# Kernel tuning notes

Measured on AMD Instinct MI355X. Metric: run time of the kernel, lower is better.

The kernel has to match this reference:

```python
import jax, jax.numpy as jnp
import numpy as np

N = 50000
E = 600000
IN_C = 128
OUT_C = 64
HID = 2 * OUT_C  # 128


def setup_inputs() -> dict:
    key = jax.random.key(0)
    ks = jax.random.split(key, 8)
    x = jax.random.normal(ks[0], (N, IN_C), dtype=jnp.float32)
    edge_index = jax.random.randint(ks[1], (2, E), 0, N, dtype=jnp.int64)
    # Glorot-style init for GCN weights, zero bias (PyG default)
    def glorot(k, fan_in, fan_out):
        s = jnp.sqrt(6.0 / (fan_in + fan_out)).astype(jnp.float32)
        return jax.random.uniform(k, (fan_in, fan_out), jnp.float32, -s, s)
    return {
        "x": x,
        "edge_index": edge_index,
        "W1": glorot(ks[2], IN_C, HID),
        "b1": jnp.zeros((HID,), jnp.float32),
        "W_mu": glorot(ks[3], HID, OUT_C),
        "b_mu": jnp.zeros((OUT_C,), jnp.float32),
        "W_ls": glorot(ks[4], HID, OUT_C),
        "b_ls": jnp.zeros((OUT_C,), jnp.float32),
    }


def _gcn_norm(edge_index, num_nodes):
    # Add self-loops, compute symmetric normalization (cached=True in original
    # means this is computed once and reused by all three convs -- same math).
    loop = jnp.arange(num_nodes, dtype=edge_index.dtype)
    row = jnp.concatenate([edge_index[0], loop])  # source
    col = jnp.concatenate([edge_index[1], loop])  # target
    deg = jax.ops.segment_sum(jnp.ones_like(col, dtype=jnp.float32), col,
                              num_segments=num_nodes)
    dis = jnp.where(deg > 0, jax.lax.rsqrt(deg), 0.0)  # deg^{-1/2}, inf->0
    norm = dis[row] * dis[col]  # [E+N]
    return row, col, norm


def _gcn_conv(x, W, b, row, col, norm, num_nodes):
    h = x @ W                                  # dense transform [N, out]
    msg = h[row] * norm[:, None]               # gather + scale [E+N, out]
    out = jax.ops.segment_sum(msg, col, num_segments=num_nodes)
    return out + b


def reference(x, edge_index, W1, b1, W_mu, b_mu, W_ls, b_ls):
    num_nodes = x.shape[0]
    row, col, norm = _gcn_norm(edge_index, num_nodes)
    # eval mode: F.dropout is identity when not training
    h = jax.nn.relu(_gcn_conv(x, W1, b1, row, col, norm, num_nodes))
    mu = _gcn_conv(h, W_mu, b_mu, row, col, norm, num_nodes)
    logstd = _gcn_conv(h, W_ls, b_ls, row, col, norm, num_nodes)
    return mu, logstd
```

## Files before the change

kernel.cpp:

```cpp
#include <hip/hip_runtime.h>
#include <hip/hip_fp16.h>


#define N_NODES 50000
#define N_EDGES 600000
#define MU_SIZE (N_NODES * 64)
#define SCAN_BLOCKS 200
#define SCAN_CHUNK 250
#define WT_S 136

typedef _Float16 half8 __attribute__((ext_vector_type(8)));
typedef _Float16 half4 __attribute__((ext_vector_type(4)));
typedef float floatx4 __attribute__((ext_vector_type(4)));

union H8 { __half2 h2[4]; float4 f4; };

__global__ __launch_bounds__(256) void count_kernel(const int* __restrict__ col,
                                                    int* __restrict__ counts, int e) {
  int i = blockIdx.x * 256 + threadIdx.x;
  if (i < e) atomicAdd(&counts[col[i]], 1);
}

__global__ __launch_bounds__(256) void blocksum_dis_kernel(const int* __restrict__ counts,
                                                           float* __restrict__ dis,
                                                           int* __restrict__ blocksums) {
  __shared__ int red[4];
  int b = blockIdx.x, t = threadIdx.x;
  int i = b * SCAN_CHUNK + t;
  int c = 0;
  if (t < SCAN_CHUNK) {
    c = counts[i];
    dis[i] = rsqrtf((float)(c + 1));
  }
  int s = c;
#pragma unroll
  for (int off = 32; off > 0; off >>= 1) s += __shfl_down(s, off, 64);
  if ((t & 63) == 0) red[t >> 6] = s;
  __syncthreads();
  if (t == 0) blocksums[b] = red[0] + red[1] + red[2] + red[3];
}

__global__ __launch_bounds__(256) void offsets_kernel(const int* __restrict__ counts,
                                                      const int* __restrict__ blocksums,
                                                      int* __restrict__ offsets) {
  __shared__ int sb[256];
  __shared__ int loc[256];
  int b = blockIdx.x, t = threadIdx.x;
  sb[t] = (t < SCAN_BLOCKS) ? blocksums[t] : 0;
  __syncthreads();
#pragma unroll
  for (int off = 1; off < 256; off <<= 1) {
    int v = (t >= off) ? sb[t - off] : 0;
    __syncthreads();
    sb[t] += v;
    __syncthreads();
  }
  int base = (b == 0) ? 0 : sb[b - 1];
  int i = b * SCAN_CHUNK + t;
  int c = (t < SCAN_CHUNK) ? counts[i] : 0;
  loc[t] = c;
  __syncthreads();
#pragma unroll
  for (int off = 1; off < 256; off <<= 1) {
    int v = (t >= off) ? loc[t - off] : 0;
    __syncthreads();
    loc[t] += v;
    __syncthreads();
  }
  if (t < SCAN_CHUNK) offsets[i] = base + loc[t] - c;
  if (b == SCAN_BLOCKS - 1 && t == SCAN_CHUNK - 1) offsets[N_NODES] = base + loc[t];
}

__global__ __launch_bounds__(256) void fill_kernel(const int* __restrict__ row,
                                                   const int* __restrict__ col,
                                                   const int* __restrict__ offsets,
                                                   int* __restrict__ fillcnt,
                                                   int* __restrict__ srcidx, int e) {
  int i = blockIdx.x * 256 + threadIdx.x;
  if (i < e) {
    int c = col[i];
    int pos = offsets[c] + atomicAdd(&fillcnt[c], 1);
    srcidx[pos] = row[i];
  }
}

__global__ __launch_bounds__(256) void prep_wt_kernel(const float* __restrict__ W1,
                                                      const float* __restrict__ Wmu,
                                                      const float* __restrict__ Wls,
                                                      _Float16* __restrict__ W1T,
                                                      _Float16* __restrict__ W2T) {
  int idx = blockIdx.x * 256 + threadIdx.x;
  int e = idx & 16383;
  int n = e >> 7, k = e & 127;
  if (idx < 16384) {
    W1T[e] = (_Float16)W1[k * 128 + n];
  } else {
    float w = (n < 64) ? Wmu[k * 64 + n] : Wls[k * 64 + (n - 64)];
    W2T[e] = (_Float16)w;
  }
}

template <bool SPLIT>
__global__ __launch_bounds__(256) void gemm_mfma_kernel(const float* __restrict__ X,
                                                        const _Float16* __restrict__ Xh,
                                                        const _Float16* __restrict__ WT,
                                                        const float* __restrict__ dis,
                                                        const float* __restrict__ ba,
                                                        const float* __restrict__ bb,
                                                        _Float16* __restrict__ Yh,
                                                        float* __restrict__ Yf) {
  __shared__ _Float16 WL[128 * WT_S];

  int t = threadIdx.x;
  for (int idx = t; idx < 128 * 16; idx += 256) {
    int n = idx >> 4, kk = (idx & 15) * 8;
    *(half8*)&WL[n * WT_S + kk] = *(const half8*)&WT[n * 128 + kk];
  }
  __syncthreads();

  int wid = t >> 6, lane = t & 63;
  int q = lane >> 4, m = lane & 15;
  const int ngroups = (N_NODES + 63) / 64;

  for (int g64 = blockIdx.x; g64 < ngroups; g64 += gridDim.x) {
    int node = g64 * 64 + wid * 16 + m;
    size_t nr = (size_t)min(node, N_NODES - 1);
    bool valid = node < N_NODES;

    half8 xfrag[4];
    if (!SPLIT) {
#pragma unroll
      for (int c = 0; c < 4; ++c) {
        const float* ap = &X[nr * 128 + 32 * c + 8 * q];
        float4 a0 = *(const float4*)ap;
        float4 a1 = *(const float4*)(ap + 4);
        half8 af = {(_Float16)a0.x, (_Float16)a0.y, (_Float16)a0.z, (_Float16)a0.w,
                    (_Float16)a1.x, (_Float16)a1.y, (_Float16)a1.z, (_Float16)a1.w};
        xfrag[c] = af;
      }
    } else {
#pragma unroll
      for (int c = 0; c < 4; ++c) {
        xfrag[c] = *(const half8*)&Xh[nr * 128 + 32 * c + 8 * q];
      }
    }
    float dnode = SPLIT ? 0.f : dis[nr];

#pragma unroll
    for (int f = 0; f < 8; ++f) {
      floatx4 acc = {0.f, 0.f, 0.f, 0.f};
#pragma unroll
      for (int c = 0; c < 4; ++c) {
        half8 wfrag = *(const half8*)&WL[(16 * f + m) * WT_S + 32 * c + 8 * q];
        acc = __builtin_amdgcn_mfma_f32_16x16x32_f16(wfrag, xfrag[c], acc, 0, 0, 0);
      }
      int fbase = 16 * f + 4 * q;
      if (!SPLIT) {
        if (valid) {
          half4 o = {(_Float16)(acc[0] * dnode), (_Float16)(acc[1] * dnode),
                     (_Float16)(acc[2] * dnode), (_Float16)(acc[3] * dnode)};
          *(half4*)&Yh[(size_t)node * 128 + fbase] = o;
        }
      } else {
        float4 bias = (f < 4) ? *(const float4*)&ba[fbase]
                              : *(const float4*)&bb[fbase - 64];
        float4 o = make_float4(acc[0] + bias.x, acc[1] + bias.y, acc[2] + bias.z,
                               acc[3] + bias.w);
        if (valid) {
          if (f < 4)
            *(float4*)&Yf[(size_t)node * 64 + fbase] = o;
          else
            *(float4*)&Yf[MU_SIZE + (size_t)node * 64 + (fbase - 64)] = o;
        }
      }
    }
  }
}

template <bool BIAS_RELU>
__global__ __launch_bounds__(256) void aggregate_kernel(const __half* __restrict__ Hs,
                                                        const int* __restrict__ offsets,
                                                        const int* __restrict__ srcidx,
                                                        const float* __restrict__ dis,
                                                        const float* __restrict__ bias,
                                                        __half* __restrict__ outH, int n) {
  int wid = threadIdx.x >> 6, lane = threadIdx.x & 63;
  int q = lane >> 4, ql = lane & 15;
  int i = blockIdx.x * 16 + wid * 4 + q;
  if (i >= n) return;
  float di = dis[i];
  float4 selfv = ((const float4*)(Hs + (size_t)i * 128))[ql];
  float acc[8] = {0.f, 0.f, 0.f, 0.f, 0.f, 0.f, 0.f, 0.f};
  int k = offsets[i], end = offsets[i + 1];
  for (; k + 3 < end; k += 4) {
    int r0 = srcidx[k];
    int r1 = srcidx[k + 1];
    int r2 = srcidx[k + 2];
    int r3 = srcidx[k + 3];
    float4 v0 = ((const float4*)(Hs + (size_t)r0 * 128))[ql];
    float4 v1 = ((const float4*)(Hs + (size_t)r1 * 128))[ql];
    float4 v2 = ((const float4*)(Hs + (size_t)r2 * 128))[ql];
    float4 v3 = ((const float4*)(Hs + (size_t)r3 * 128))[ql];
    const __half2* a0 = (const __half2*)&v0;
    const __half2* a1 = (const __half2*)&v1;
    const __half2* a2 = (const __half2*)&v2;
    const __half2* a3 = (const __half2*)&v3;
#pragma unroll
    for (int j = 0; j < 4; ++j) {
      float2 f0 = __half22float2(a0[j]);
      float2 f1 = __half22float2(a1[j]);
      float2 f2 = __half22float2(a2[j]);
      float2 f3 = __half22float2(a3[j]);
      acc[2 * j] += (f0.x + f1.x) + (f2.x + f3.x);
      acc[2 * j + 1] += (f0.y + f1.y) + (f2.y + f3.y);
    }
  }
  for (; k < end; ++k) {
    int r0 = srcidx[k];
    float4 v0 = ((const float4*)(Hs + (size_t)r0 * 128))[ql];
    const __half2* a0 = (const __half2*)&v0;
#pragma unroll
    for (int j = 0; j < 4; ++j) {
      float2 f0 = __half22float2(a0[j]);
      acc[2 * j] += f0.x;
      acc[2 * j + 1] += f0.y;
    }
  }
  const __half2* sh = (const __half2*)&selfv;
  float s[8];
#pragma unroll
  for (int j = 0; j < 4; ++j) {
    float2 f = __half22float2(sh[j]);
    s[2 * j] = di * (acc[2 * j] + f.x);
    s[2 * j + 1] = di * (acc[2 * j + 1] + f.y);
  }
  H8 u;
  if (BIAS_RELU) {
    float4 b0 = ((const float4*)bias)[2 * ql];
    float4 b1 = ((const float4*)bias)[2 * ql + 1];
    u.h2[0] = __float22half2_rn(
        make_float2(di * fmaxf(s[0] + b0.x, 0.f), di * fmaxf(s[1] + b0.y, 0.f)));
    u.h2[1] = __float22half2_rn(
        make_float2(di * fmaxf(s[2] + b0.z, 0.f), di * fmaxf(s[3] + b0.w, 0.f)));
    u.h2[2] = __float22half2_rn(
        make_float2(di * fmaxf(s[4] + b1.x, 0.f), di * fmaxf(s[5] + b1.y, 0.f)));
    u.h2[3] = __float22half2_rn(
        make_float2(di * fmaxf(s[6] + b1.z, 0.f), di * fmaxf(s[7] + b1.w, 0.f)));
  } else {
    u.h2[0] = __float22half2_rn(make_float2(s[0], s[1]));
    u.h2[1] = __float22half2_rn(make_float2(s[2], s[3]));
    u.h2[2] = __float22half2_rn(make_float2(s[4], s[5]));
    u.h2[3] = __float22half2_rn(make_float2(s[6], s[7]));
  }
  ((float4*)(outH + (size_t)i * 128))[ql] = u.f4;
}

extern "C" void kernel_launch(void* const* d_in, const int* in_sizes, int n_in,
                              void* d_out, int out_size, void* d_ws, size_t ws_size,
                              hipStream_t stream) {
  const float* x = (const float*)d_in[0];
  const int* ei = (const int*)d_in[1];
  const float* W1 = (const float*)d_in[2];
  const float* b1 = (const float*)d_in[3];
  const float* Wmu = (const float*)d_in[4];
  const float* bmu = (const float*)d_in[5];
  const float* Wls = (const float*)d_in[6];
  const float* bls = (const float*)d_in[7];
  float* out = (float*)d_out;

  const int* row = ei;
  const int* col = ei + N_EDGES;

  __half* bufAh = (__half*)d_ws;
  __half* bufBh = bufAh + 6400000;
  __half* bufCh = bufBh + 6400000;
  float* dis = (float*)(bufCh + 6400000);
  int* counts = (int*)(dis + N_NODES);
  int* fillcnt = counts + N_NODES;
  int* offsets = fillcnt + N_NODES;
  int* srcidx = offsets + N_NODES + 1;
  int* blocksums = srcidx + N_EDGES;
  _Float16* W1T = (_Float16*)(blocksums + 256);
  _Float16* W2T = W1T + 16384;

  hipMemsetAsync(counts, 0, 2 * N_NODES * sizeof(int), stream);

  prep_wt_kernel<<<128, 256, 0, stream>>>(W1, Wmu, Wls, W1T, W2T);

  int eb = (N_EDGES + 255) / 256;
  count_kernel<<<eb, 256, 0, stream>>>(col, counts, N_EDGES);
  blocksum_dis_kernel<<<SCAN_BLOCKS, 256, 0, stream>>>(counts, dis, blocksums);
  offsets_kernel<<<SCAN_BLOCKS, 256, 0, stream>>>(counts, blocksums, offsets);
  fill_kernel<<<eb, 256, 0, stream>>>(row, col, offsets, fillcnt, srcidx, N_EDGES);

  gemm_mfma_kernel<false><<<512, 256, 0, stream>>>(x, nullptr, W1T, dis, nullptr, nullptr,
                                                   (_Float16*)bufAh, nullptr);
  int ab = (N_NODES + 15) / 16;
  aggregate_kernel<true><<<ab, 256, 0, stream>>>(bufAh, offsets, srcidx, dis, b1,
                                                 bufBh, N_NODES);
  aggregate_kernel<false><<<ab, 256, 0, stream>>>(bufBh, offsets, srcidx, dis,
                                                  nullptr, bufCh, N_NODES);
  gemm_mfma_kernel<true><<<512, 256, 0, stream>>>(nullptr, (const _Float16*)bufCh, W2T,
                                                  nullptr, bmu, bls, nullptr, out);
}
```

Baseline: 222.1 us.

## Split fp16 feature buffers into four 32-channel planes for cache-local aggregation

Stores the intermediate fp16 node features as four planes of 32 channels (64 bytes per node) instead of 128-channel rows, and launches the aggregation with four blocks per node group, one per plane. Each gather then touches a smaller per-plane working set (3.2 MB), so the random neighbour reads are meant to hit L2/MALL more often. The GEMM producer and consumer are changed to read and write the planar layout. In exchange, the CSR index lists are read four times, each lane issues narrow 4-byte loads, and there are four times as many blocks.

```diff
diff --git a/kernel.cpp b/kernel.cpp
--- a/kernel.cpp
+++ b/kernel.cpp
@@ -8,12 +8,11 @@
 #define SCAN_BLOCKS 200
 #define SCAN_CHUNK 250
 #define WT_S 136
+#define PLANE (N_NODES * 32)
 
 typedef _Float16 half8 __attribute__((ext_vector_type(8)));
 typedef _Float16 half4 __attribute__((ext_vector_type(4)));
 typedef float floatx4 __attribute__((ext_vector_type(4)));
-
-union H8 { __half2 h2[4]; float4 f4; };
 
 __global__ __launch_bounds__(256) void count_kernel(const int* __restrict__ col,
                                                     int* __restrict__ counts, int e) {
@@ -141,7 +140,7 @@
     } else {
 #pragma unroll
       for (int c = 0; c < 4; ++c) {
-        xfrag[c] = *(const half8*)&Xh[nr * 128 + 32 * c + 8 * q];
+        xfrag[c] = *(const half8*)&Xh[(size_t)c * PLANE + nr * 32 + 8 * q];
       }
     }
     float dnode = SPLIT ? 0.f : dis[nr];
@@ -159,7 +158,8 @@
         if (valid) {
           half4 o = {(_Float16)(acc[0] * dnode), (_Float16)(acc[1] * dnode),
                      (_Float16)(acc[2] * dnode), (_Float16)(acc[3] * dnode)};
-          *(half4*)&Yh[(size_t)node * 128 + fbase] = o;
+          int p = fbase >> 5, c0 = fbase & 31;
+          *(half4*)&Yh[(size_t)p * PLANE + (size_t)node * 32 + c0] = o;
         }
       } else {
         float4 bias = (f < 4) ? *(const float4*)&ba[fbase]
@@ -184,75 +184,54 @@
                                                         const float* __restrict__ dis,
                                                         const float* __restrict__ bias,
                                                         __half* __restrict__ outH, int n) {
+  int bid = blockIdx.x;
+  int p = bid & 3;
+  int nb = bid >> 2;
   int wid = threadIdx.x >> 6, lane = threadIdx.x & 63;
   int q = lane >> 4, ql = lane & 15;
-  int i = blockIdx.x * 16 + wid * 4 + q;
+  int i = nb * 16 + wid * 4 + q;
   if (i >= n) return;
+  const __half* plane = Hs + (size_t)p * PLANE;
   float di = dis[i];
-  float4 selfv = ((const float4*)(Hs + (size_t)i * 128))[ql];
-  float acc[8] = {0.f, 0.f, 0.f, 0.f, 0.f, 0.f, 0.f, 0.f};
+  __half2 selfv = *(const __half2*)(plane + (size_t)i * 32 + 2 * ql);
+  float ax = 0.f, ay = 0.f;
   int k = offsets[i], end = offsets[i + 1];
-  for (; k + 3 < end; k += 4) {
-    int r0 = srcidx[k];
-    int r1 = srcidx[k + 1];
-    int r2 = srcidx[k + 2];
-    int r3 = srcidx[k + 3];
-    float4 v0 = ((const float4*)(Hs + (size_t)r0 * 128))[ql];
-    float4 v1 = ((const float4*)(Hs + (size_t)r1 * 128))[ql];
-    float4 v2 = ((const float4*)(Hs + (size_t)r2 * 128))[ql];
-    float4 v3 = ((const float4*)(Hs + (size_t)r3 * 128))[ql];
-    const __half2* a0 = (const __half2*)&v0;
-    const __half2* a1 = (const __half2*)&v1;
-    const __half2* a2 = (const __half2*)&v2;
-    const __half2* a3 = (const __half2*)&v3;
-#pragma unroll
-    for (int j = 0; j < 4; ++j) {
-      float2 f0 = __half22float2(a0[j]);
-      float2 f1 = __half22float2(a1[j]);
-      float2 f2 = __half22float2(a2[j]);
-      float2 f3 = __half22float2(a3[j]);
-      acc[2 * j] += (f0.x + f1.x) + (f2.x + f3.x);
-      acc[2 * j + 1] += (f0.y + f1.y) + (f2.y + f3.y);
-    }
+  for (; k + 7 < end; k += 8) {
+    int r0 = srcidx[k], r1 = srcidx[k + 1], r2 = srcidx[k + 2], r3 = srcidx[k + 3];
+    int r4 = srcidx[k + 4], r5 = srcidx[k + 5], r6 = srcidx[k + 6], r7 = srcidx[k + 7];
+    __half2 v0 = *(const __half2*)(plane + (size_t)r0 * 32 + 2 * ql);
+    __half2 v1 = *(const __half2*)(plane + (size_t)r1 * 32 + 2 * ql);
+    __half2 v2 = *(const __half2*)(plane + (size_t)r2 * 32 + 2 * ql);
+    __half2 v3 = *(const __half2*)(plane + (size_t)r3 * 32 + 2 * ql);
+    __half2 v4 = *(const __half2*)(plane + (size_t)r4 * 32 + 2 * ql);
+    __half2 v5 = *(const __half2*)(plane + (size_t)r5 * 32 + 2 * ql);
+    __half2 v6 = *(const __half2*)(plane + (size_t)r6 * 32 + 2 * ql);
+    __half2 v7 = *(const __half2*)(plane + (size_t)r7 * 32 + 2 * ql);
+    float2 f0 = __half22float2(v0), f1 = __half22float2(v1);
+    float2 f2 = __half22float2(v2), f3 = __half22float2(v3);
+    float2 f4 = __half22float2(v4), f5 = __half22float2(v5);
+    float2 f6 = __half22float2(v6), f7 = __half22float2(v7);
+    ax += ((f0.x + f1.x) + (f2.x + f3.x)) + ((f4.x + f5.x) + (f6.x + f7.x));
+    ay += ((f0.y + f1.y) + (f2.y + f3.y)) + ((f4.y + f5.y) + (f6.y + f7.y));
   }
   for (; k < end; ++k) {
     int r0 = srcidx[k];
-    float4 v0 = ((const float4*)(Hs + (size_t)r0 * 128))[ql];
-    const __half2* a0 = (const __half2*)&v0;
-#pragma unroll
-    for (int j = 0; j < 4; ++j) {
-      float2 f0 = __half22float2(a0[j]);
-      acc[2 * j] += f0.x;
-      acc[2 * j + 1] += f0.y;
-    }
-  }
-  const __half2* sh = (const __half2*)&selfv;
-  float s[8];
-#pragma unroll
-  for (int j = 0; j < 4; ++j) {
-    float2 f = __half22float2(sh[j]);
-    s[2 * j] = di * (acc[2 * j] + f.x);
-    s[2 * j + 1] = di * (acc[2 * j + 1] + f.y);
-  }
-  H8 u;
+    float2 f0 = __half22float2(*(const __half2*)(plane + (size_t)r0 * 32 + 2 * ql));
+    ax += f0.x;
+    ay += f0.y;
+  }
+  float2 sf = __half22float2(selfv);
+  float sx = di * (ax + sf.x);
+  float sy = di * (ay + sf.y);
+  __half2 o;
   if (BIAS_RELU) {
-    float4 b0 = ((const float4*)bias)[2 * ql];
-    float4 b1 = ((const float4*)bias)[2 * ql + 1];
-    u.h2[0] = __float22half2_rn(
-        make_float2(di * fmaxf(s[0] + b0.x, 0.f), di * fmaxf(s[1] + b0.y, 0.f)));
-    u.h2[1] = __float22half2_rn(
-        make_float2(di * fmaxf(s[2] + b0.z, 0.f), di * fmaxf(s[3] + b0.w, 0.f)));
-    u.h2[2] = __float22half2_rn(
-        make_float2(di * fmaxf(s[4] + b1.x, 0.f), di * fmaxf(s[5] + b1.y, 0.f)));
-    u.h2[3] = __float22half2_rn(
-        make_float2(di * fmaxf(s[6] + b1.z, 0.f), di * fmaxf(s[7] + b1.w, 0.f)));
+    float2 b = *(const float2*)&bias[p * 32 + 2 * ql];
+    o = __float22half2_rn(
+        make_float2(di * fmaxf(sx + b.x, 0.f), di * fmaxf(sy + b.y, 0.f)));
   } else {
-    u.h2[0] = __float22half2_rn(make_float2(s[0], s[1]));
-    u.h2[1] = __float22half2_rn(make_float2(s[2], s[3]));
-    u.h2[2] = __float22half2_rn(make_float2(s[4], s[5]));
-    u.h2[3] = __float22half2_rn(make_float2(s[6], s[7]));
-  }
-  ((float4*)(outH + (size_t)i * 128))[ql] = u.f4;
+    o = __float22half2_rn(make_float2(sx, sy));
+  }
+  *(__half2*)(outH + (size_t)p * PLANE + (size_t)i * 32 + 2 * ql) = o;
 }
 
 extern "C" void kernel_launch(void* const* d_in, const int* in_sizes, int n_in,
@@ -296,10 +275,10 @@
   gemm_mfma_kernel<false><<<512, 256, 0, stream>>>(x, nullptr, W1T, dis, nullptr, nullptr,
                                                    (_Float16*)bufAh, nullptr);
   int ab = (N_NODES + 15) / 16;
-  aggregate_kernel<true><<<ab, 256, 0, stream>>>(bufAh, offsets, srcidx, dis, b1,
-                                                 bufBh, N_NODES);
-  aggregate_kernel<false><<<ab, 256, 0, stream>>>(bufBh, offsets, srcidx, dis,
-                                                  nullptr, bufCh, N_NODES);
+  aggregate_kernel<true><<<4 * ab, 256, 0, stream>>>(bufAh, offsets, srcidx, dis, b1,
+                                                     bufBh, N_NODES);
+  aggregate_kernel<false><<<4 * ab, 256, 0, stream>>>(bufBh, offsets, srcidx, dis,
+                                                      nullptr, bufCh, N_NODES);
   gemm_mfma_kernel<true><<<512, 256, 0, stream>>>(nullptr, (const _Float16*)bufCh, W2T,
                                                   nullptr, bmu, bls, nullptr, out);
 }
```

Measured after the change: 245.7 us. 1.11x slower.

## Fuse second aggregation with final GEMM and fold memset into weight prep

Applied to the files above, without the earlier changes.

The second sparse aggregation now writes its fp16 result into shared memory, and the same block runs the MFMA GEMM for mu/logstd. This drops one intermediate buffer's global write and read plus a kernel launch. The memset of the counters is folded into the weight-prep kernel, removing another launch. In exchange, each block loads the weight tile into LDS for only 64 nodes and uses more shared memory, which may lower occupancy for the gather phase.

```diff
diff --git a/kernel.cpp b/kernel.cpp
--- a/kernel.cpp
+++ b/kernel.cpp
@@ -88,8 +88,10 @@
                                                       const float* __restrict__ Wmu,
                                                       const float* __restrict__ Wls,
                                                       _Float16* __restrict__ W1T,
-                                                      _Float16* __restrict__ W2T) {
+                                                      _Float16* __restrict__ W2T,
+                                                      int* __restrict__ zero2n) {
   int idx = blockIdx.x * 256 + threadIdx.x;
+  for (int z = idx; z < 2 * N_NODES; z += 32768) zero2n[z] = 0;
   int e = idx & 16383;
   int n = e >> 7, k = e & 127;
   if (idx < 16384) {
@@ -100,15 +102,10 @@
   }
 }
 
-template <bool SPLIT>
-__global__ __launch_bounds__(256) void gemm_mfma_kernel(const float* __restrict__ X,
-                                                        const _Float16* __restrict__ Xh,
-                                                        const _Float16* __restrict__ WT,
-                                                        const float* __restrict__ dis,
-                                                        const float* __restrict__ ba,
-                                                        const float* __restrict__ bb,
-                                                        _Float16* __restrict__ Yh,
-                                                        float* __restrict__ Yf) {
+__global__ __launch_bounds__(256) void gemm1_kernel(const float* __restrict__ X,
+                                                    const _Float16* __restrict__ WT,
+                                                    const float* __restrict__ dis,
+                                                    _Float16* __restrict__ Yh) {
   __shared__ _Float16 WL[128 * WT_S];
 
   int t = threadIdx.x;
@@ -128,23 +125,16 @@
     bool valid = node < N_NODES;
 
     half8 xfrag[4];
-    if (!SPLIT) {
-#pragma unroll
-      for (int c = 0; c < 4; ++c) {
-        const float* ap = &X[nr * 128 + 32 * c + 8 * q];
-        float4 a0 = *(const float4*)ap;
-        float4 a1 = *(const float4*)(ap + 4);
-        half8 af = {(_Float16)a0.x, (_Float16)a0.y, (_Float16)a0.z, (_Float16)a0.w,
-                    (_Float16)a1.x, (_Float16)a1.y, (_Float16)a1.z, (_Float16)a1.w};
-        xfrag[c] = af;
-      }
-    } else {
-#pragma unroll
-      for (int c = 0; c < 4; ++c) {
-        xfrag[c] = *(const half8*)&Xh[nr * 128 + 32 * c + 8 * q];
-      }
-    }
-    float dnode = SPLIT ? 0.f : dis[nr];
+#pragma unroll
+    for (int c = 0; c < 4; ++c) {
+      const float* ap = &X[nr * 128 + 32 * c + 8 * q];
+      float4 a0 = *(const float4*)ap;
+      float4 a1 = *(const float4*)(ap + 4);
+      half8 af = {(_Float16)a0.x, (_Float16)a0.y, (_Float16)a0.z, (_Float16)a0.w,
+                  (_Float16)a1.x, (_Float16)a1.y, (_Float16)a1.z, (_Float16)a1.w};
+      xfrag[c] = af;
+    }
+    float dnode = dis[nr];
 
 #pragma unroll
     for (int f = 0; f < 8; ++f) {
@@ -154,44 +144,19 @@
         half8 wfrag = *(const half8*)&WL[(16 * f + m) * WT_S + 32 * c + 8 * q];
         acc = __builtin_amdgcn_mfma_f32_16x16x32_f16(wfrag, xfrag[c], acc, 0, 0, 0);
       }
-      int fbase = 16 * f + 4 * q;
-      if (!SPLIT) {
-        if (valid) {
-          half4 o = {(_Float16)(acc[0] * dnode), (_Float16)(acc[1] * dnode),
-                     (_Float16)(acc[2] * dnode), (_Float16)(acc[3] * dnode)};
-          *(half4*)&Yh[(size_t)node * 128 + fbase] = o;
-        }
-      } else {
-        float4 bias = (f < 4) ? *(const float4*)&ba[fbase]
-                              : *(const float4*)&bb[fbase - 64];
-        float4 o = make_float4(acc[0] + bias.x, acc[1] + bias.y, acc[2] + bias.z,
-                               acc[3] + bias.w);
-        if (valid) {
-          if (f < 4)
-            *(float4*)&Yf[(size_t)node * 64 + fbase] = o;
-          else
-            *(float4*)&Yf[MU_SIZE + (size_t)node * 64 + (fbase - 64)] = o;
-        }
+      if (valid) {
+        int fbase = 16 * f + 4 * q;
+        half4 o = {(_Float16)(acc[0] * dnode), (_Float16)(acc[1] * dnode),
+                   (_Float16)(acc[2] * dnode), (_Float16)(acc[3] * dnode)};
+        *(half4*)&Yh[(size_t)node * 128 + fbase] = o;
       }
     }
   }
 }
 
-template <bool BIAS_RELU>
-__global__ __launch_bounds__(256) void aggregate_kernel(const __half* __restrict__ Hs,
-                                                        const int* __restrict__ offsets,
-                                                        const int* __restrict__ srcidx,
-                                                        const float* __restrict__ dis,
-                                                        const float* __restrict__ bias,
-                                                        __half* __restrict__ outH, int n) {
-  int wid = threadIdx.x >> 6, lane = threadIdx.x & 63;
-  int q = lane >> 4, ql = lane & 15;
-  int i = blockIdx.x * 16 + wid * 4 + q;
-  if (i >= n) return;
-  float di = dis[i];
-  float4 selfv = ((const float4*)(Hs + (size_t)i * 128))[ql];
-  float acc[8] = {0.f, 0.f, 0.f, 0.f, 0.f, 0.f, 0.f, 0.f};
-  int k = offsets[i], end = offsets[i + 1];
+__device__ inline void gather_sum(const __half* __restrict__ Hs,
+                                  const int* __restrict__ srcidx, int k, int end,
+                                  int ql, float acc[8]) {
   for (; k + 3 < end; k += 4) {
     int r0 = srcidx[k];
     int r1 = srcidx[k + 1];
@@ -226,33 +191,112 @@
       acc[2 * j + 1] += f0.y;
     }
   }
+}
+
+__global__ __launch_bounds__(256) void aggregate_relu_kernel(
+    const __half* __restrict__ Hs, const int* __restrict__ offsets,
+    const int* __restrict__ srcidx, const float* __restrict__ dis,
+    const float* __restrict__ bias, __half* __restrict__ outH, int n) {
+  int wid = threadIdx.x >> 6, lane = threadIdx.x & 63;
+  int q = lane >> 4, ql = lane & 15;
+  int i = blockIdx.x * 16 + wid * 4 + q;
+  if (i >= n) return;
+  float di = dis[i];
+  float4 selfv = ((const float4*)(Hs + (size_t)i * 128))[ql];
+  float acc[8] = {0.f, 0.f, 0.f, 0.f, 0.f, 0.f, 0.f, 0.f};
+  gather_sum(Hs, srcidx, offsets[i], offsets[i + 1], ql, acc);
   const __half2* sh = (const __half2*)&selfv;
-  float s[8];
-#pragma unroll
-  for (int j = 0; j < 4; ++j) {
-    float2 f = __half22float2(sh[j]);
-    s[2 * j] = di * (acc[2 * j] + f.x);
-    s[2 * j + 1] = di * (acc[2 * j + 1] + f.y);
-  }
+  float4 b0 = ((const float4*)bias)[2 * ql];
+  float4 b1 = ((const float4*)bias)[2 * ql + 1];
   H8 u;
-  if (BIAS_RELU) {
-    float4 b0 = ((const float4*)bias)[2 * ql];
-    float4 b1 = ((const float4*)bias)[2 * ql + 1];
-    u.h2[0] = __float22half2_rn(
-        make_float2(di * fmaxf(s[0] + b0.x, 0.f), di * fmaxf(s[1] + b0.y, 0.f)));
-    u.h2[1] = __float22half2_rn(
-        make_float2(di * fmaxf(s[2] + b0.z, 0.f), di * fmaxf(s[3] + b0.w, 0.f)));
-    u.h2[2] = __float22half2_rn(
-        make_float2(di * fmaxf(s[4] + b1.x, 0.f), di * fmaxf(s[5] + b1.y, 0.f)));
-    u.h2[3] = __float22half2_rn(
-        make_float2(di * fmaxf(s[6] + b1.z, 0.f), di * fmaxf(s[7] + b1.w, 0.f)));
-  } else {
-    u.h2[0] = __float22half2_rn(make_float2(s[0], s[1]));
-    u.h2[1] = __float22half2_rn(make_float2(s[2], s[3]));
-    u.h2[2] = __float22half2_rn(make_float2(s[4], s[5]));
-    u.h2[3] = __float22half2_rn(make_float2(s[6], s[7]));
-  }
+  float2 f0 = __half22float2(sh[0]);
+  float2 f1 = __half22float2(sh[1]);
+  float2 f2 = __half22float2(sh[2]);
+  float2 f3 = __half22float2(sh[3]);
+  float s0 = di * (acc[0] + f0.x), s1 = di * (acc[1] + f0.y);
+  float s2 = di * (acc[2] + f1.x), s3 = di * (acc[3] + f1.y);
+  float s4 = di * (acc[4] + f2.x), s5 = di * (acc[5] + f2.y);
+  float s6 = di * (acc[6] + f3.x), s7 = di * (acc[7] + f3.y);
+  u.h2[0] = __float22half2_rn(
+      make_float2(di * fmaxf(s0 + b0.x, 0.f), di * fmaxf(s1 + b0.y, 0.f)));
+  u.h2[1] = __float22half2_rn(
+      make_float2(di * fmaxf(s2 + b0.z, 0.f), di * fmaxf(s3 + b0.w, 0.f)));
+  u.h2[2] = __float22half2_rn(
+      make_float2(di * fmaxf(s4 + b1.x, 0.f), di * fmaxf(s5 + b1.y, 0.f)));
+  u.h2[3] = __float22half2_rn(
+      make_float2(di * fmaxf(s6 + b1.z, 0.f), di * fmaxf(s7 + b1.w, 0.f)));
   ((float4*)(outH + (size_t)i * 128))[ql] = u.f4;
+}
+
+__global__ __launch_bounds__(256) void agg_gemm_kernel(
+    const __half* __restrict__ Hs, const int* __restrict__ offsets,
+    const int* __restrict__ srcidx, const float* __restrict__ dis,
+    const _Float16* __restrict__ WT, const float* __restrict__ ba,
+    const float* __restrict__ bb, float* __restrict__ Yf) {
+  __shared__ _Float16 WL[128 * WT_S];
+  __shared__ _Float16 HL[64 * WT_S];
+
+  int t = threadIdx.x;
+  for (int idx = t; idx < 128 * 16; idx += 256) {
+    int n = idx >> 4, kk = (idx & 15) * 8;
+    *(half8*)&WL[n * WT_S + kk] = *(const half8*)&WT[n * 128 + kk];
+  }
+  __syncthreads();
+
+  int wid = t >> 6, lane = t & 63;
+  int q = lane >> 4, ql = lane & 15;
+  int base = blockIdx.x * 64 + wid * 16;
+
+#pragma unroll 1
+  for (int s = 0; s < 4; ++s) {
+    int i = base + q * 4 + s;
+    if (i < N_NODES) {
+      float di = dis[i];
+      float4 selfv = ((const float4*)(Hs + (size_t)i * 128))[ql];
+      float acc[8] = {0.f, 0.f, 0.f, 0.f, 0.f, 0.f, 0.f, 0.f};
+      gather_sum(Hs, srcidx, offsets[i], offsets[i + 1], ql, acc);
+      const __half2* sh = (const __half2*)&selfv;
+      H8 u;
+#pragma unroll
+      for (int j = 0; j < 4; ++j) {
+        float2 f = __half22float2(sh[j]);
+        u.h2[j] = __float22half2_rn(
+            make_float2(di * (acc[2 * j] + f.x), di * (acc[2 * j + 1] + f.y)));
+      }
+      *(float4*)&HL[(wid * 16 + q * 4 + s) * WT_S + 8 * ql] = u.f4;
+    }
+  }
+
+  int m = lane & 15;
+  int node = base + m;
+  bool valid = node < N_NODES;
+
+  half8 xfrag[4];
+#pragma unroll
+  for (int c = 0; c < 4; ++c) {
+    xfrag[c] = *(const half8*)&HL[(wid * 16 + m) * WT_S + 32 * c + 8 * q];
+  }
+
+#pragma unroll
+  for (int f = 0; f < 8; ++f) {
+    floatx4 acc = {0.f, 0.f, 0.f, 0.f};
+#pragma unroll
+    for (int c = 0; c < 4; ++c) {
+      half8 wfrag = *(const half8*)&WL[(16 * f + m) * WT_S + 32 * c + 8 * q];
+      acc = __builtin_amdgcn_mfma_f32_16x16x32_f16(wfrag, xfrag[c], acc, 0, 0, 0);
+    }
+    int fbase = 16 * f + 4 * q;
+    float4 bias = (f < 4) ? *(const float4*)&ba[fbase]
+                          : *(const float4*)&bb[fbase - 64];
+    float4 o = make_float4(acc[0] + bias.x, acc[1] + bias.y, acc[2] + bias.z,
+                           acc[3] + bias.w);
+    if (valid) {
+      if (f < 4)
+        *(float4*)&Yf[(size_t)node * 64 + fbase] = o;
+      else
+        *(float4*)&Yf[MU_SIZE + (size_t)node * 64 + (fbase - 64)] = o;
+    }
+  }
 }
 
 extern "C" void kernel_launch(void* const* d_in, const int* in_sizes, int n_in,
@@ -273,8 +317,7 @@
 
   __half* bufAh = (__half*)d_ws;
   __half* bufBh = bufAh + 6400000;
-  __half* bufCh = bufBh + 6400000;
-  float* dis = (float*)(bufCh + 6400000);
+  float* dis = (float*)(bufBh + 6400000);
   int* counts = (int*)(dis + N_NODES);
   int* fillcnt = counts + N_NODES;
   int* offsets = fillcnt + N_NODES;
@@ -283,9 +326,7 @@
   _Float16* W1T = (_Float16*)(blocksums + 256);
   _Float16* W2T = W1T + 16384;
 
-  hipMemsetAsync(counts, 0, 2 * N_NODES * sizeof(int), stream);
-
-  prep_wt_kernel<<<128, 256, 0, stream>>>(W1, Wmu, Wls, W1T, W2T);
+  prep_wt_kernel<<<128, 256, 0, stream>>>(W1, Wmu, Wls, W1T, W2T, counts);
 
   int eb = (N_EDGES + 255) / 256;
   count_kernel<<<eb, 256, 0, stream>>>(col, counts, N_EDGES);
@@ -293,13 +334,11 @@
   offsets_kernel<<<SCAN_BLOCKS, 256, 0, stream>>>(counts, blocksums, offsets);
   fill_kernel<<<eb, 256, 0, stream>>>(row, col, offsets, fillcnt, srcidx, N_EDGES);
 
-  gemm_mfma_kernel<false><<<512, 256, 0, stream>>>(x, nullptr, W1T, dis, nullptr, nullptr,
-                                                   (_Float16*)bufAh, nullptr);
+  gemm1_kernel<<<512, 256, 0, stream>>>(x, W1T, dis, (_Float16*)bufAh);
   int ab = (N_NODES + 15) / 16;
-  aggregate_kernel<true><<<ab, 256, 0, stream>>>(bufAh, offsets, srcidx, dis, b1,
-                                                 bufBh, N_NODES);
-  aggregate_kernel<false><<<ab, 256, 0, stream>>>(bufBh, offsets, srcidx, dis,
-                                                  nullptr, bufCh, N_NODES);
-  gemm_mfma_kernel<true><<<512, 256, 0, stream>>>(nullptr, (const _Float16*)bufCh, W2T,
-                                                  nullptr, bmu, bls, nullptr, out);
-}
+  aggregate_relu_kernel<<<ab, 256, 0, stream>>>(bufAh, offsets, srcidx, dis, b1,
+                                                bufBh, N_NODES);
+  int fb = (N_NODES + 63) / 64;
+  agg_gemm_kernel<<<fb, 256, 0, stream>>>(bufBh, offsets, srcidx, dis, W2T, bmu, bls,
+                                          out);
+}
```

Result: slower. 239.2 us (+7.7%).

## Pad CSR neighbor lists to multiples of eight with zero-row sentinel

Applied to the files above, without the earlier changes.

Each node's in-degree is rounded up to a multiple of eight in the offset scan. The unused slots point to an extra all-zero feature row appended to each half-precision buffer, so the aggregation loop can gather eight rows per iteration with no remainder loop. The memset is folded into the weight-prep kernel, which also fills the padded index array and zeroes the sentinel rows. This removes the scalar tail loop and increases memory-level parallelism per wavefront. The cost is extra sentinel gathers (up to seven per node) and a larger index array to initialise.

```diff
diff --git a/kernel.cpp b/kernel.cpp
--- a/kernel.cpp
+++ b/kernel.cpp
@@ -8,6 +8,7 @@
 #define SCAN_BLOCKS 200
 #define SCAN_CHUNK 250
 #define WT_S 136
+#define PAD_CAP 960000
 
 typedef _Float16 half8 __attribute__((ext_vector_type(8)));
 typedef _Float16 half4 __attribute__((ext_vector_type(4)));
@@ -27,12 +28,13 @@
   __shared__ int red[4];
   int b = blockIdx.x, t = threadIdx.x;
   int i = b * SCAN_CHUNK + t;
-  int c = 0;
+  int dp = 0;
   if (t < SCAN_CHUNK) {
-    c = counts[i];
+    int c = counts[i];
     dis[i] = rsqrtf((float)(c + 1));
-  }
-  int s = c;
+    dp = (c + 7) & ~7;
+  }
+  int s = dp;
 #pragma unroll
   for (int off = 32; off > 0; off >>= 1) s += __shfl_down(s, off, 64);
   if ((t & 63) == 0) red[t >> 6] = s;
@@ -57,8 +59,9 @@
   }
   int base = (b == 0) ? 0 : sb[b - 1];
   int i = b * SCAN_CHUNK + t;
-  int c = (t < SCAN_CHUNK) ? counts[i] : 0;
-  loc[t] = c;
+  int dp = 0;
+  if (t < SCAN_CHUNK) dp = (counts[i] + 7) & ~7;
+  loc[t] = dp;
   __syncthreads();
 #pragma unroll
   for (int off = 1; off < 256; off <<= 1) {
@@ -67,7 +70,7 @@
     loc[t] += v;
     __syncthreads();
   }
-  if (t < SCAN_CHUNK) offsets[i] = base + loc[t] - c;
+  if (t < SCAN_CHUNK) offsets[i] = base + loc[t] - dp;
   if (b == SCAN_BLOCKS - 1 && t == SCAN_CHUNK - 1) offsets[N_NODES] = base + loc[t];
 }
 
@@ -84,12 +87,22 @@
   }
 }
 
-__global__ __launch_bounds__(256) void prep_wt_kernel(const float* __restrict__ W1,
-                                                      const float* __restrict__ Wmu,
-                                                      const float* __restrict__ Wls,
-                                                      _Float16* __restrict__ W1T,
-                                                      _Float16* __restrict__ W2T) {
+__global__ __launch_bounds__(256) void prep_kernel(const float* __restrict__ W1,
+                                                   const float* __restrict__ Wmu,
+                                                   const float* __restrict__ Wls,
+                                                   _Float16* __restrict__ W1T,
+                                                   _Float16* __restrict__ W2T,
+                                                   int* __restrict__ zero2n,
+                                                   int* __restrict__ srcidx,
+                                                   __half* __restrict__ zrowA,
+                                                   __half* __restrict__ zrowB) {
   int idx = blockIdx.x * 256 + threadIdx.x;
+  for (int z = idx; z < 2 * N_NODES; z += 32768) zero2n[z] = 0;
+  for (int z = idx; z < PAD_CAP; z += 32768) srcidx[z] = N_NODES;
+  if (idx < 128) {
+    zrowA[idx] = __float2half(0.f);
+    zrowB[idx] = __float2half(0.f);
+  }
   int e = idx & 16383;
   int n = e >> 7, k = e & 127;
   if (idx < 16384) {
@@ -192,65 +205,65 @@
   float4 selfv = ((const float4*)(Hs + (size_t)i * 128))[ql];
   float acc[8] = {0.f, 0.f, 0.f, 0.f, 0.f, 0.f, 0.f, 0.f};
   int k = offsets[i], end = offsets[i + 1];
-  for (; k + 3 < end; k += 4) {
-    int r0 = srcidx[k];
-    int r1 = srcidx[k + 1];
-    int r2 = srcidx[k + 2];
-    int r3 = srcidx[k + 3];
+  for (; k < end; k += 8) {
+    int r0 = srcidx[k], r1 = srcidx[k + 1], r2 = srcidx[k + 2], r3 = srcidx[k + 3];
+    int r4 = srcidx[k + 4], r5 = srcidx[k + 5], r6 = srcidx[k + 6], r7 = srcidx[k + 7];
     float4 v0 = ((const float4*)(Hs + (size_t)r0 * 128))[ql];
     float4 v1 = ((const float4*)(Hs + (size_t)r1 * 128))[ql];
     float4 v2 = ((const float4*)(Hs + (size_t)r2 * 128))[ql];
     float4 v3 = ((const float4*)(Hs + (size_t)r3 * 128))[ql];
+    float4 v4 = ((const float4*)(Hs + (size_t)r4 * 128))[ql];
+    float4 v5 = ((const float4*)(Hs + (size_t)r5 * 128))[ql];
+    float4 v6 = ((const float4*)(Hs + (size_t)r6 * 128))[ql];
+    float4 v7 = ((const float4*)(Hs + (size_t)r7 * 128))[ql];
     const __half2* a0 = (const __half2*)&v0;
     const __half2* a1 = (const __half2*)&v1;
     const __half2* a2 = (const __half2*)&v2;
     const __half2* a3 = (const __half2*)&v3;
+    const __half2* a4 = (const __half2*)&v4;
+    const __half2* a5 = (const __half2*)&v5;
+    const __half2* a6 = (const __half2*)&v6;
+    const __half2* a7 = (const __half2*)&v7;
 #pragma unroll
     for (int j = 0; j < 4; ++j) {
       float2 f0 = __half22float2(a0[j]);
       float2 f1 = __half22float2(a1[j]);
       float2 f2 = __half22float2(a2[j]);
       float2 f3 = __half22float2(a3[j]);
-      acc[2 * j] += (f0.x + f1.x) + (f2.x + f3.x);
-      acc[2 * j + 1] += (f0.y + f1.y) + (f2.y + f3.y);
+      float2 f4 = __half22float2(a4[j]);
+      float2 f5 = __half22float2(a5[j]);
+      float2 f6 = __half22float2(a6[j]);
+      float2 f7 = __half22float2(a7[j]);
+      acc[2 * j] += ((f0.x + f1.x) + (f2.x + f3.x)) + ((f4.x + f5.x) + (f6.x + f7.x));
+      acc[2 * j + 1] += ((f0.y + f1.y) + (f2.y + f3.y)) + ((f4.y + f5.y) + (f6.y + f7.y));
     }
   }
-  for (; k < end; ++k) {
-    int r0 = srcidx[k];
-    float4 v0 = ((const float4*)(Hs + (size_t)r0 * 128))[ql];
-    const __half2* a0 = (const __half2*)&v0;
-#pragma unroll
-    for (int j = 0; j < 4; ++j) {
-      float2 f0 = __half22float2(a0[j]);
-      acc[2 * j] += f0.x;
-      acc[2 * j + 1] += f0.y;
-    }
-  }
   const __half2* sh = (const __half2*)&selfv;
-  float s[8];
-#pragma unroll
-  for (int j = 0; j < 4; ++j) {
-    float2 f = __half22float2(sh[j]);
-    s[2 * j] = di * (acc[2 * j] + f.x);
-    s[2 * j + 1] = di * (acc[2 * j + 1] + f.y);
-  }
+  float2 f0 = __half22float2(sh[0]);
+  float2 f1 = __half22float2(sh[1]);
+  float2 f2 = __half22float2(sh[2]);
+  float2 f3 = __half22float2(sh[3]);
+  float s0 = di * (acc[0] + f0.x), s1 = di * (acc[1] + f0.y);
+  float s2 = di * (acc[2] + f1.x), s3 = di * (acc[3] + f1.y);
+  float s4 = di * (acc[4] + f2.x), s5 = di * (acc[5] + f2.y);
+  float s6 = di * (acc[6] + f3.x), s7 = di * (acc[7] + f3.y);
   H8 u;
   if (BIAS_RELU) {
     float4 b0 = ((const float4*)bias)[2 * ql];
     float4 b1 = ((const float4*)bias)[2 * ql + 1];
     u.h2[0] = __float22half2_rn(
-        make_float2(di * fmaxf(s[0] + b0.x, 0.f), di * fmaxf(s[1] + b0.y, 0.f)));
+        make_float2(di * fmaxf(s0 + b0.x, 0.f), di * fmaxf(s1 + b0.y, 0.f)));
     u.h2[1] = __float22half2_rn(
-        make_float2(di * fmaxf(s[2] + b0.z, 0.f), di * fmaxf(s[3] + b0.w, 0.f)));
+        make_float2(di * fmaxf(s2 + b0.z, 0.f), di * fmaxf(s3 + b0.w, 0.f)));
     u.h2[2] = __float22half2_rn(
-        make_float2(di * fmaxf(s[4] + b1.x, 0.f), di * fmaxf(s[5] + b1.y, 0.f)));
+        make_float2(di * fmaxf(s4 + b1.x, 0.f), di * fmaxf(s5 + b1.y, 0.f)));
     u.h2[3] = __float22half2_rn(
-        make_float2(di * fmaxf(s[6] + b1.z, 0.f), di * fmaxf(s[7] + b1.w, 0.f)));
+        make_float2(di * fmaxf(s6 + b1.z, 0.f), di * fmaxf(s7 + b1.w, 0.f)));
   } else {
-    u.h2[0] = __float22half2_rn(make_float2(s[0], s[1]));
-    u.h2[1] = __float22half2_rn(make_float2(s[2], s[3]));
-    u.h2[2] = __float22half2_rn(make_float2(s[4], s[5]));
-    u.h2[3] = __float22half2_rn(make_float2(s[6], s[7]));
+    u.h2[0] = __float22half2_rn(make_float2(s0, s1));
+    u.h2[1] = __float22half2_rn(make_float2(s2, s3));
+    u.h2[2] = __float22half2_rn(make_float2(s4, s5));
+    u.h2[3] = __float22half2_rn(make_float2(s6, s7));
   }
   ((float4*)(outH + (size_t)i * 128))[ql] = u.f4;
 }
@@ -272,20 +285,20 @@
   const int* col = ei + N_EDGES;
 
   __half* bufAh = (__half*)d_ws;
-  __half* bufBh = bufAh + 6400000;
-  __half* bufCh = bufBh + 6400000;
+  __half* bufBh = bufAh + 6400128;
+  __half* bufCh = bufBh + 6400128;
   float* dis = (float*)(bufCh + 6400000);
   int* counts = (int*)(dis + N_NODES);
   int* fillcnt = counts + N_NODES;
   int* offsets = fillcnt + N_NODES;
   int* srcidx = offsets + N_NODES + 1;
-  int* blocksums = srcidx + N_EDGES;
+  int* blocksums = srcidx + PAD_CAP;
   _Float16* W1T = (_Float16*)(blocksums + 256);
   _Float16* W2T = W1T + 16384;
 
-  hipMemsetAsync(counts, 0, 2 * N_NODES * sizeof(int), stream);
-
-  prep_wt_kernel<<<128, 256, 0, stream>>>(W1, Wmu, Wls, W1T, W2T);
+  prep_kernel<<<128, 256, 0, stream>>>(W1, Wmu, Wls, W1T, W2T, counts, srcidx,
+                                       bufAh + (size_t)N_NODES * 128,
+                                       bufBh + (size_t)N_NODES * 128);
 
   int eb = (N_EDGES + 255) / 256;
   count_kernel<<<eb, 256, 0, stream>>>(col, counts, N_EDGES);
```

After: 218.6 us. No clear change (-1.6%).
